# Kernel optimization log

Measured on AMD Instinct MI355X. Metric: run time of the kernel, lower is better.

## Reference

```python
import jax, jax.numpy as jnp
import numpy as np

N_STARS = 2048   # n_stars
BATCH = 256      # query positions per call
PF = 28          # poly_features = (d_max+1)(d_max+2)/2, d_max=6
NGE = 512        # n_graph_elems
GF = 32          # graph_features
OPD = 256        # opd_dim


def setup_inputs() -> dict:
    key = jax.random.key(0)
    ks = jax.random.split(key, 8)
    # observed star positions in the FoV (x_lims/y_lims = [0,1000])
    obs_pos = jax.random.uniform(ks[0], (N_STARS, 2), jnp.float32, 0.0, 1000.0)
    # query positions are exact rows of obs_pos (required by the exact-match index search)
    idx = jax.random.randint(ks[1], (BATCH,), 0, N_STARS)
    positions = obs_pos[idx]
    poly_dic = jax.random.normal(ks[2], (N_STARS, PF), jnp.float32)
    graph_dic = jax.random.normal(ks[3], (N_STARS, NGE), jnp.float32)
    # alpha matrices: identity(-padded) init as in init_vars, plus small noise
    alpha_poly = jnp.eye(PF, dtype=jnp.float32) + 0.01 * jax.random.normal(ks[4], (PF, PF), jnp.float32)
    alpha_graph = (jnp.eye(NGE, GF, dtype=jnp.float32)
                   + 0.01 * jax.random.normal(ks[5], (NGE, GF), jnp.float32))
    # S features: random uniform in [-1e-3, 1e-3] as in init_vars
    S_poly = jax.random.uniform(ks[6], (PF, OPD, OPD), jnp.float32, -0.001, 0.001)
    S_graph = jax.random.uniform(ks[7], (GF, OPD, OPD), jnp.float32, -0.001, 0.001)
    return {
        'positions': positions, 'obs_pos': obs_pos,
        'poly_dic': poly_dic, 'graph_dic': graph_dic,
        'alpha_poly': alpha_poly, 'alpha_graph': alpha_graph,
        'S_poly': S_poly, 'S_graph': S_graph,
    }


def _calc_indices(positions, obs_pos):
    # Faithful to tf.where(tf.equal(obs_pos, pos))[0, 0]: first True entry (row-major)
    # of the elementwise equality over (n_stars, 2); its row index is taken.
    eq = positions[:, None, :] == obs_pos[None, :, :]          # (B, N, 2) bool
    flat_first = jnp.argmax(eq.reshape(eq.shape[0], -1), axis=1)  # first True, flat index
    return flat_first // 2                                      # row index in obs_pos


def reference(positions, obs_pos, poly_dic, graph_dic, alpha_poly, alpha_graph, S_poly, S_graph):
    indices = _calc_indices(positions, obs_pos)                 # (B,) int
    # polynomial part: gather -> matmul -> tensordot with OPD modes
    batch_poly = jnp.take(poly_dic, indices, axis=0)            # (B, PF)
    interm_poly = batch_poly @ alpha_poly                       # (B, PF)
    contrib_poly = jnp.einsum('bp,pij->bij', interm_poly, S_poly)  # (B, OPD, OPD)
    # graph part
    batch_graph = jnp.take(graph_dic, indices, axis=0)          # (B, NGE)
    interm_graph = batch_graph @ alpha_graph                    # (B, GF)
    contrib_graph = jnp.einsum('bg,gij->bij', interm_graph, S_graph)
    return contrib_poly + contrib_graph
```

## Files before the change

### kernel.cpp

```cpp
#include <hip/hip_runtime.h>

#define NSTARS 2048
#define BATCH  256
#define PF     28
#define NGE    512
#define GF     32
#define OPD2   65536
#define KTOT   (PF + GF)
#define TM     32

__global__ __launch_bounds__(256) void prep_kernel(
    const float* __restrict__ positions,  const float* __restrict__ obs_pos,
    const float* __restrict__ poly_dic,   const float* __restrict__ graph_dic,
    const float* __restrict__ alpha_poly, const float* __restrict__ alpha_graph,
    float* __restrict__ Wt)
{
    const int b = blockIdx.x;
    const int t = threadIdx.x;

    const float p0 = positions[2 * b];
    const float p1 = positions[2 * b + 1];

    int cand = 0x7fffffff;
    #pragma unroll
    for (int i = 0; i < NSTARS / 256; ++i) {
        const int n = t + i * 256;
        const float o0 = obs_pos[2 * n];
        const float o1 = obs_pos[2 * n + 1];
        if (o0 == p0 || o1 == p1) cand = min(cand, n);
    }
    __shared__ int smin[256];
    smin[t] = cand;
    __syncthreads();
    for (int s = 128; s > 0; s >>= 1) {
        if (t < s) smin[t] = min(smin[t], smin[t + s]);
        __syncthreads();
    }
    int idx = smin[0];
    if (idx == 0x7fffffff) idx = 0;

    if (t < PF) {
        float acc = 0.f;
        #pragma unroll
        for (int p = 0; p < PF; ++p)
            acc += poly_dic[idx * PF + p] * alpha_poly[p * PF + t];
        Wt[t * BATCH + b] = acc;
    }

    __shared__ float psum[8][GF];
    {
        const int g = t & 31;
        const int r = t >> 5;
        float acc = 0.f;
        const int e0 = r * (NGE / 8);
        for (int e = e0; e < e0 + NGE / 8; ++e)
            acc += graph_dic[idx * NGE + e] * alpha_graph[e * GF + g];
        psum[r][g] = acc;
    }
    __syncthreads();
    if (t < GF) {
        float acc = 0.f;
        #pragma unroll
        for (int r = 0; r < 8; ++r) acc += psum[r][t];
        Wt[(PF + t) * BATCH + b] = acc;
    }
}

__global__ __launch_bounds__(256) void main_kernel(
    const float* __restrict__ S_poly, const float* __restrict__ S_graph,
    const float* __restrict__ Wt, float* __restrict__ out)
{
    const int t  = threadIdx.x;
    const int ij = blockIdx.x * 1024 + t * 4;
    const int b0 = blockIdx.y * TM;

    float4 acc[TM];
    #pragma unroll
    for (int b = 0; b < TM; ++b) acc[b] = make_float4(0.f, 0.f, 0.f, 0.f);

    const float* __restrict__ wp = Wt + b0;

    #pragma unroll 2
    for (int k = 0; k < PF; ++k) {
        const float4 s = *reinterpret_cast<const float4*>(
            S_poly + (size_t)k * OPD2 + ij);
        #pragma unroll
        for (int b = 0; b < TM; ++b) {
            const float w = wp[k * BATCH + b];
            acc[b].x += w * s.x;
            acc[b].y += w * s.y;
            acc[b].z += w * s.z;
            acc[b].w += w * s.w;
        }
    }
    #pragma unroll 2
    for (int k = 0; k < GF; ++k) {
        const float4 s = *reinterpret_cast<const float4*>(
            S_graph + (size_t)k * OPD2 + ij);
        #pragma unroll
        for (int b = 0; b < TM; ++b) {
            const float w = wp[(PF + k) * BATCH + b];
            acc[b].x += w * s.x;
            acc[b].y += w * s.y;
            acc[b].z += w * s.z;
            acc[b].w += w * s.w;
        }
    }

    #pragma unroll
    for (int b = 0; b < TM; ++b) {
        *reinterpret_cast<float4*>(out + (size_t)(b0 + b) * OPD2 + ij) = acc[b];
    }
}

extern "C" void kernel_launch(void* const* d_in, const int* in_sizes, int n_in,
                              void* d_out, int out_size, void* d_ws, size_t ws_size,
                              hipStream_t stream) {
    const float* positions   = (const float*)d_in[0];
    const float* obs_pos     = (const float*)d_in[1];
    const float* poly_dic    = (const float*)d_in[2];
    const float* graph_dic   = (const float*)d_in[3];
    const float* alpha_poly  = (const float*)d_in[4];
    const float* alpha_graph = (const float*)d_in[5];
    const float* S_poly      = (const float*)d_in[6];
    const float* S_graph     = (const float*)d_in[7];
    float* out = (float*)d_out;

    float* Wt = (float*)d_ws;

    prep_kernel<<<BATCH, 256, 0, stream>>>(positions, obs_pos, poly_dic,
                                           graph_dic, alpha_poly, alpha_graph,
                                           Wt);

    dim3 grid(OPD2 / 1024, BATCH / TM);
    main_kernel<<<grid, 256, 0, stream>>>(S_poly, S_graph, Wt, out);
}
```

Measured before the change: 126.6 us.

## Use bf16 MFMA with split-precision weights for the S contraction

Replaces the FP32 FMA main kernel with a matrix-core path. S is converted each call into bf16 in an MFMA fragment layout, and the weight matrix is split into bf16 hi and lo parts so accuracy is partly kept. Blocks are swizzled across XCDs, and outputs use nontemporal stores. This adds two conversion kernels and an extra pass over S, and S itself is rounded to bf16, which risks precision loss against the reference. A smaller-tile FP32 fallback runs when the workspace is too small.

Result: faster. 123.3 us (-2.5%).

```diff
diff --git a/kernel.cpp b/kernel.cpp
--- a/kernel.cpp
+++ b/kernel.cpp
@@ -7,7 +7,17 @@
 #define GF     32
 #define OPD2   65536
 #define KTOT   (PF + GF)
-#define TM     32
+#define NTILE  4096
+
+#define WA_OFF 61440
+#define WA_HALF 32768
+#define SB_OFF (WA_OFF + 2 * WA_HALF)
+#define SB_BYTES ((size_t)NTILE * 2 * 64 * 16)
+#define WS_NEED (SB_OFF + SB_BYTES)
+
+typedef float f32x4 __attribute__((ext_vector_type(4)));
+typedef short bf16x8 __attribute__((ext_vector_type(8)));
+typedef unsigned int u32;
 
 __global__ __launch_bounds__(256) void prep_kernel(
     const float* __restrict__ positions,  const float* __restrict__ obs_pos,
@@ -66,51 +76,148 @@
     }
 }
 
-__global__ __launch_bounds__(256) void main_kernel(
+__device__ __forceinline__ u32 bf16_rne(u32 x) {
+    return (x + 0x7FFFu + ((x >> 16) & 1u)) >> 16;
+}
+__device__ __forceinline__ float bf16_to_f32(u32 h) {
+    return __uint_as_float(h << 16);
+}
+
+__global__ __launch_bounds__(256) void prep2_kernel(
+    const float* __restrict__ Wt, u32* __restrict__ Wa_hi, u32* __restrict__ Wa_lo)
+{
+    const int f     = blockIdx.x * 256 + threadIdx.x;
+    const int lane  = f & 63;
+    const int kf    = (f >> 6) & 1;
+    const int mtile = f >> 7;
+    const int m     = mtile * 16 + (lane & 15);
+    const int kbase = kf * 32 + (lane >> 4) * 8;
+    u32 hi_pk[4], lo_pk[4];
+    #pragma unroll
+    for (int p = 0; p < 4; ++p) {
+        u32 h[2], l[2];
+        #pragma unroll
+        for (int q = 0; q < 2; ++q) {
+            const int k = kbase + 2 * p + q;
+            float w = (k < KTOT) ? Wt[k * BATCH + m] : 0.f;
+            const u32 hb = bf16_rne(__float_as_uint(w));
+            const float resid = w - bf16_to_f32(hb);
+            h[q] = hb;
+            l[q] = bf16_rne(__float_as_uint(resid));
+        }
+        hi_pk[p] = h[0] | (h[1] << 16);
+        lo_pk[p] = l[0] | (l[1] << 16);
+    }
+    *reinterpret_cast<f32x4*>(Wa_hi + f * 4) = *reinterpret_cast<f32x4*>(hi_pk);
+    *reinterpret_cast<f32x4*>(Wa_lo + f * 4) = *reinterpret_cast<f32x4*>(lo_pk);
+}
+
+__global__ __launch_bounds__(256) void conv_kernel(
+    const float* __restrict__ S_poly, const float* __restrict__ S_graph,
+    u32* __restrict__ Sb)
+{
+    const int f    = blockIdx.x * 256 + threadIdx.x;
+    const int lane = f & 63;
+    const int kf   = (f >> 6) & 1;
+    const int tile = f >> 7;
+    const int ij   = tile * 16 + (lane & 15);
+    const int kbase = kf * 32 + (lane >> 4) * 8;
+    u32 pk[4];
+    #pragma unroll
+    for (int p = 0; p < 4; ++p) {
+        u32 b16[2];
+        #pragma unroll
+        for (int q = 0; q < 2; ++q) {
+            const int k = kbase + 2 * p + q;
+            u32 v = 0u;
+            if (k < KTOT) {
+                const float s = (k < PF) ? S_poly[(size_t)k * OPD2 + ij]
+                                         : S_graph[(size_t)(k - PF) * OPD2 + ij];
+                v = bf16_rne(__float_as_uint(s));
+            }
+            b16[q] = v;
+        }
+        pk[p] = b16[0] | (b16[1] << 16);
+    }
+    *reinterpret_cast<f32x4*>(Sb + (size_t)f * 4) = *reinterpret_cast<f32x4*>(pk);
+}
+
+__global__ __launch_bounds__(256) void mfma_kernel(
+    const u32* __restrict__ Sb, const u32* __restrict__ Wa_hi,
+    const u32* __restrict__ Wa_lo, float* __restrict__ out)
+{
+    const int t    = threadIdx.x;
+    const int id   = blockIdx.x;
+    const int xcd  = id & 7;
+    const int slot = id >> 3;
+    const int xb   = xcd * 32 + (slot & 31);
+    const int yb   = slot >> 5;
+    const int w    = t >> 6;
+    const int lane = t & 63;
+    const int b0   = yb * 64;
+    const int Tb   = xb * 16 + w * 4;
+
+    bf16x8 Ah[4][2], Al[4][2];
+    #pragma unroll
+    for (int mt = 0; mt < 4; ++mt)
+        #pragma unroll
+        for (int kf = 0; kf < 2; ++kf) {
+            const int fi = (((yb * 4 + mt) * 2 + kf) * 64 + lane) * 4;
+            Ah[mt][kf] = *reinterpret_cast<const bf16x8*>(Wa_hi + fi);
+            Al[mt][kf] = *reinterpret_cast<const bf16x8*>(Wa_lo + fi);
+        }
+
+    const int row = (lane >> 4) * 4;
+    const int col = lane & 15;
+
+    #pragma unroll
+    for (int tt = 0; tt < 4; ++tt) {
+        const int T = Tb + tt;
+        const bf16x8 B0 = *reinterpret_cast<const bf16x8*>(
+            Sb + ((size_t)(T * 2 + 0) * 64 + lane) * 4);
+        const bf16x8 B1 = *reinterpret_cast<const bf16x8*>(
+            Sb + ((size_t)(T * 2 + 1) * 64 + lane) * 4);
+        #pragma unroll
+        for (int mt = 0; mt < 4; ++mt) {
+            f32x4 acc = (f32x4)(0.f);
+            acc = __builtin_amdgcn_mfma_f32_16x16x32_bf16(Al[mt][0], B0, acc, 0, 0, 0);
+            acc = __builtin_amdgcn_mfma_f32_16x16x32_bf16(Al[mt][1], B1, acc, 0, 0, 0);
+            acc = __builtin_amdgcn_mfma_f32_16x16x32_bf16(Ah[mt][0], B0, acc, 0, 0, 0);
+            acc = __builtin_amdgcn_mfma_f32_16x16x32_bf16(Ah[mt][1], B1, acc, 0, 0, 0);
+            float* op = out + (size_t)(b0 + mt * 16 + row) * OPD2 + T * 16 + col;
+            #pragma unroll
+            for (int j = 0; j < 4; ++j)
+                __builtin_nontemporal_store(acc[j], op + (size_t)j * OPD2);
+        }
+    }
+}
+
+__global__ __launch_bounds__(256) void fb_kernel(
     const float* __restrict__ S_poly, const float* __restrict__ S_graph,
     const float* __restrict__ Wt, float* __restrict__ out)
 {
     const int t  = threadIdx.x;
     const int ij = blockIdx.x * 1024 + t * 4;
-    const int b0 = blockIdx.y * TM;
-
-    float4 acc[TM];
-    #pragma unroll
-    for (int b = 0; b < TM; ++b) acc[b] = make_float4(0.f, 0.f, 0.f, 0.f);
-
+    const int b0 = blockIdx.y * 16;
+    f32x4 acc[16];
+    #pragma unroll
+    for (int b = 0; b < 16; ++b) acc[b] = (f32x4)(0.f);
     const float* __restrict__ wp = Wt + b0;
-
     #pragma unroll 2
     for (int k = 0; k < PF; ++k) {
-        const float4 s = *reinterpret_cast<const float4*>(
-            S_poly + (size_t)k * OPD2 + ij);
-        #pragma unroll
-        for (int b = 0; b < TM; ++b) {
-            const float w = wp[k * BATCH + b];
-            acc[b].x += w * s.x;
-            acc[b].y += w * s.y;
-            acc[b].z += w * s.z;
-            acc[b].w += w * s.w;
-        }
+        const f32x4 s = *reinterpret_cast<const f32x4*>(S_poly + (size_t)k * OPD2 + ij);
+        #pragma unroll
+        for (int b = 0; b < 16; ++b) acc[b] += wp[k * BATCH + b] * s;
     }
     #pragma unroll 2
     for (int k = 0; k < GF; ++k) {
-        const float4 s = *reinterpret_cast<const float4*>(
-            S_graph + (size_t)k * OPD2 + ij);
-        #pragma unroll
-        for (int b = 0; b < TM; ++b) {
-            const float w = wp[(PF + k) * BATCH + b];
-            acc[b].x += w * s.x;
-            acc[b].y += w * s.y;
-            acc[b].z += w * s.z;
-            acc[b].w += w * s.w;
-        }
-    }
-
-    #pragma unroll
-    for (int b = 0; b < TM; ++b) {
-        *reinterpret_cast<float4*>(out + (size_t)(b0 + b) * OPD2 + ij) = acc[b];
-    }
+        const f32x4 s = *reinterpret_cast<const f32x4*>(S_graph + (size_t)k * OPD2 + ij);
+        #pragma unroll
+        for (int b = 0; b < 16; ++b) acc[b] += wp[(PF + k) * BATCH + b] * s;
+    }
+    #pragma unroll
+    for (int b = 0; b < 16; ++b)
+        *reinterpret_cast<f32x4*>(out + (size_t)(b0 + b) * OPD2 + ij) = acc[b];
 }
 
 extern "C" void kernel_launch(void* const* d_in, const int* in_sizes, int n_in,
@@ -132,6 +239,15 @@
                                            graph_dic, alpha_poly, alpha_graph,
                                            Wt);
 
-    dim3 grid(OPD2 / 1024, BATCH / TM);
-    main_kernel<<<grid, 256, 0, stream>>>(S_poly, S_graph, Wt, out);
-}
+    if (ws_size >= WS_NEED) {
+        u32* Wa_hi = (u32*)((char*)d_ws + WA_OFF);
+        u32* Wa_lo = (u32*)((char*)d_ws + WA_OFF + WA_HALF);
+        u32* Sb    = (u32*)((char*)d_ws + SB_OFF);
+        prep2_kernel<<<8, 256, 0, stream>>>(Wt, Wa_hi, Wa_lo);
+        conv_kernel<<<2048, 256, 0, stream>>>(S_poly, S_graph, Sb);
+        mfma_kernel<<<1024, 256, 0, stream>>>(Sb, Wa_hi, Wa_lo, out);
+    } else {
+        dim3 grid(OPD2 / 1024, BATCH / 16);
+        fb_kernel<<<grid, 256, 0, stream>>>(S_poly, S_graph, Wt, out);
+    }
+}
```
